# Performance work log

Hardware: AMD Instinct MI355X
Metric: run time of the kernel (lower is better)

## Reference

```python
import jax, jax.numpy as jnp
import numpy as np

BS, N, D, NC = 64, 512, 256, 4
REG = 0.5
N_ITER = 10
BIG = 1.0e9
LN_EPS = 1e-5


def _layer_norm(x, g, b):
    m = jnp.mean(x, axis=-1, keepdims=True)
    v = jnp.mean((x - m) ** 2, axis=-1, keepdims=True)
    return (x - m) * jax.lax.rsqrt(v + LN_EPS) * g + b


def _embed(x, W1, b1, g1, be1, W2, b2, g2, be2):
    h = _layer_norm(jax.nn.leaky_relu(x @ W1 + b1, 0.01), g1, be1)
    return _layer_norm(jax.nn.leaky_relu(h @ W2 + b2, 0.01), g2, be2)


def _one_hot_st(logits):
    # convert_one_hot(mode='max', hard=True, four_class=False, train): straight-through one-hot
    y = jax.nn.softmax(logits, axis=-1)
    y_hard = jax.nn.one_hot(jnp.argmax(y, axis=-1), logits.shape[-1], dtype=y.dtype)
    return jax.lax.stop_gradient(y_hard - y) + y


def _cdist(x, y):
    # torch.cdist p=2 (matmul form)
    sq = (jnp.sum(x * x, -1)[:, :, None] + jnp.sum(y * y, -1)[:, None, :]
          - 2.0 * jnp.einsum('bnd,bmd->bnm', x, y))
    return jnp.sqrt(jnp.maximum(sq, 0.0))


def _sinkhorn(a, b, C):
    # standard Sinkhorn-Knopp (POT sinkhorn_knopp), reg=REG, maxIter=N_ITER
    K = jnp.exp(-C / REG)
    def step(carry, _):
        u, v = carry
        v = b / (K.T @ u)
        u = a / (K @ v)
        return (u, v), None
    init = (jnp.full_like(a, 1.0 / a.shape[0]), jnp.full_like(b, 1.0 / b.shape[0]))
    (u, v), _ = jax.lax.scan(step, init, None, length=N_ITER)
    return u[:, None] * K * v[None, :]


def setup_inputs() -> dict:
    ks = jax.random.split(jax.random.key(0), 8)
    sc = 1.0 / np.sqrt(D)
    return {
        'case_A_logits': jax.random.normal(ks[0], (BS, N, NC), jnp.float32),
        'case_B_logits': jax.random.normal(ks[1], (BS, N, NC), jnp.float32),
        'case_A': jax.random.normal(ks[2], (BS, N, D), jnp.float32),
        'case_B': jax.random.normal(ks[3], (BS, N, D), jnp.float32),
        'relation_matrix': jax.random.uniform(ks[4], (BS, N, N), jnp.float32),
        'padding_mask_a': jnp.ones((BS, N), jnp.float32),
        'padding_mask_b': jnp.ones((BS, N), jnp.float32),
        'W1': jax.random.normal(ks[5], (D, D), jnp.float32) * sc,
        'b1': jnp.zeros((D,), jnp.float32),
        'g1': jnp.ones((D,), jnp.float32),
        'be1': jnp.zeros((D,), jnp.float32),
        'W2': jax.random.normal(ks[6], (D, D), jnp.float32) * sc,
        'b2': jnp.zeros((D,), jnp.float32),
        'g2': jnp.ones((D,), jnp.float32),
        'be2': jnp.zeros((D,), jnp.float32),
    }


def reference(case_A_logits, case_B_logits, case_A, case_B, relation_matrix,
              padding_mask_a, padding_mask_b,
              W1, b1, g1, be1, W2, b2, g2, be2):
    n = case_B_logits.shape[1]
    A1 = _one_hot_st(case_A_logits)                       # [bs, n, 4]
    B1 = _one_hot_st(case_B_logits)
    class_mask = jnp.einsum('bnc,bmc->bnm', A1, B1)       # [bs, n, n]
    pm = padding_mask_a[:, :, None] * padding_mask_b[:, None, :]
    pmv = -BIG * pm + BIG
    eA = _embed(case_A, W1, b1, g1, be1, W2, b2, g2, be2)
    eB = _embed(case_B, W1, b1, g1, be1, W2, b2, g2, be2)
    cost = _cdist(eA, eB)                                 # [bs, n, n]
    cost_class = cost + pmv                               # train path
    margin = jnp.full((n,), 1.0 / n, cost.dtype)
    plan = jax.vmap(lambda c: _sinkhorn(margin, margin, c))(cost_class)
    in_loss = jnp.mean(cost_class * class_mask * pm)
    out_loss = -jnp.mean(cost_class * (1.0 - class_mask) * pm)
    # simot branch: MSE criterion, simpercent=1.0 -> sim_mask all ones
    loss_raw = (plan * n - relation_matrix) ** 2
    sup_loss = jnp.sum(loss_raw * padding_mask_a[:, :, None]) / jnp.sum(padding_mask_a)
    return in_loss + out_loss + 10.0 * sup_loss
```

## Files before the change

### kernel.cpp

```cpp
#include <hip/hip_runtime.h>
#include <math.h>

#define BSZ 64
#define NPTS 512
#define DIM 256
#define MROWS 32768
#define TOTROWS 65536
#define BIGF 1.0e9f

typedef __bf16 bf16x8 __attribute__((ext_vector_type(8)));
typedef float  f32x4  __attribute__((ext_vector_type(4)));
typedef __attribute__((address_space(1))) const void* as1cv;
typedef __attribute__((address_space(3))) void* as3v;

#define KB_OFF    0ull
#define X_OFF     8388608ull
#define H_OFF     16777216ull
#define NORM_OFF  25165824ull
#define U_OFF     25231360ull
#define V_OFF     25264128ull
#define ARGA_OFF  25296896ull
#define ARGB_OFF  25329664ull
#define ACC_OFF   25362432ull
#define WT1_OFF   25362944ull
#define WT2_OFF   25395712ull

#define ACC_PA   0
#define ACC_IN   1
#define ACC_SUP  65
#define ACC_CNT  321

__device__ __forceinline__ float bf2f(unsigned short h) {
    return __uint_as_float(((unsigned int)h) << 16);
}
__device__ __forceinline__ unsigned short f2bf(float f) {
    unsigned int u = __float_as_uint(f);
    u = (u + 0x7FFFu + ((u >> 16) & 1u)) >> 16;
    return (unsigned short)u;
}

__device__ __forceinline__ float block_reduce_256(float val) {
    __shared__ float sh[4];
    int lane = threadIdx.x & 63;
    int wv = threadIdx.x >> 6;
    __syncthreads();
#pragma unroll
    for (int off = 32; off > 0; off >>= 1) val += __shfl_down(val, off, 64);
    if (lane == 0) sh[wv] = val;
    __syncthreads();
    float r = 0.f;
    if (wv == 0 && lane < 4) r = sh[lane];
    if (wv == 0) {
        r += __shfl_down(r, 2, 64);
        r += __shfl_down(r, 1, 64);
    }
    return r;
}

__device__ __forceinline__ void unpack8(uint4 w, float* k) {
    k[0] = __uint_as_float(w.x << 16);
    k[1] = __uint_as_float(w.x & 0xFFFF0000u);
    k[2] = __uint_as_float(w.y << 16);
    k[3] = __uint_as_float(w.y & 0xFFFF0000u);
    k[4] = __uint_as_float(w.z << 16);
    k[5] = __uint_as_float(w.z & 0xFFFF0000u);
    k[6] = __uint_as_float(w.w << 16);
    k[7] = __uint_as_float(w.w & 0xFFFF0000u);
}
__device__ __forceinline__ float dot8(const float* k, const float* vr) {
    float rs = k[0] * vr[0];
    rs = fmaf(k[1], vr[1], rs); rs = fmaf(k[2], vr[2], rs);
    rs = fmaf(k[3], vr[3], rs); rs = fmaf(k[4], vr[4], rs);
    rs = fmaf(k[5], vr[5], rs); rs = fmaf(k[6], vr[6], rs);
    return fmaf(k[7], vr[7], rs);
}

__device__ __forceinline__ float packed_reduce4(float p0, float p1, float p2, float p3, int l) {
    p0 += __shfl_xor(p0, 32, 64);
    p1 += __shfl_xor(p1, 32, 64);
    p2 += __shfl_xor(p2, 32, 64);
    p3 += __shfl_xor(p3, 32, 64);
    float m1 = (l & 32) ? p1 : p0;
    float m2 = (l & 32) ? p3 : p2;
    m1 += __shfl_xor(m1, 16, 64);
    m2 += __shfl_xor(m2, 16, 64);
    float s = (l & 16) ? m2 : m1;
    s += __shfl_xor(s, 8, 64);
    s += __shfl_xor(s, 4, 64);
    s += __shfl_xor(s, 2, 64);
    s += __shfl_xor(s, 1, 64);
    return s;
}
__device__ __forceinline__ float bcast_lane(float x, int lane) {
    return __uint_as_float((unsigned)__builtin_amdgcn_readlane((int)__float_as_uint(x), lane));
}

__global__ void zero_acc_kernel(float* acc, float* colsum) {
    int t = blockIdx.x * 256 + threadIdx.x;
    if (t < 512) acc[t] = 0.f;
    colsum[t] = 0.f;
}

__global__ __launch_bounds__(256) void argmax_pa_kernel(
    const float* __restrict__ la, const float* __restrict__ lb,
    const float* __restrict__ pa, int* __restrict__ argA, int* __restrict__ argB,
    float* __restrict__ acc) {
    int i = blockIdx.x * 256 + threadIdx.x;
    float4 a = *(const float4*)&la[(size_t)i * 4];
    float av[4] = {a.x, a.y, a.z, a.w};
    int ba = 0; float bv = av[0];
#pragma unroll
    for (int c = 1; c < 4; ++c) if (av[c] > bv) { bv = av[c]; ba = c; }
    argA[i] = ba;
    float4 b = *(const float4*)&lb[(size_t)i * 4];
    float bw[4] = {b.x, b.y, b.z, b.w};
    int bbi = 0; float bm = bw[0];
#pragma unroll
    for (int c = 1; c < 4; ++c) if (bw[c] > bm) { bm = bw[c]; bbi = c; }
    argB[i] = bbi;
    float p = pa[i];
#pragma unroll
    for (int off = 32; off > 0; off >>= 1) p += __shfl_down(p, off, 64);
    if ((threadIdx.x & 63) == 0) atomicAdd(&acc[ACC_PA], p);
}

__global__ __launch_bounds__(256) void cast_bf_kernel(
    const float* __restrict__ src, unsigned short* __restrict__ dst) {
    int tid = blockIdx.x * 256 + threadIdx.x;
#pragma unroll
    for (int k = 0; k < 4; ++k) {
        int i4 = tid + k * 524288;
        float4 v = *(const float4*)&src[(size_t)i4 * 4];
        ushort4 o;
        o.x = f2bf(v.x); o.y = f2bf(v.y); o.z = f2bf(v.z); o.w = f2bf(v.w);
        *(ushort4*)&dst[(size_t)i4 * 4] = o;
    }
}

__global__ __launch_bounds__(256) void cast_wt_kernel(
    const float* __restrict__ W, unsigned short* __restrict__ Wt) {
    __shared__ float tile[16][17];
    int tx = threadIdx.x & 15, ty = threadIdx.x >> 4;
    int bx = blockIdx.x, by = blockIdx.y;
    tile[ty][tx] = W[(size_t)(by * 16 + ty) * 256 + bx * 16 + tx];
    __syncthreads();
    Wt[(size_t)(bx * 16 + ty) * 256 + by * 16 + tx] = f2bf(tile[tx][ty]);
}

__global__ __launch_bounds__(256) void gemm_bf_kernel(
    const unsigned short* __restrict__ X, const unsigned short* __restrict__ Wt,
    unsigned short* __restrict__ Y) {
    __shared__ unsigned short As[64 * 256];
    __shared__ unsigned short Bs[64 * 256];
    const int t = threadIdx.x;
    const int L = t & 63, wv = t >> 6;
    const int q = L >> 4, n = L & 15;
    const size_t row0 = (size_t)blockIdx.x * 64;
    const int n0 = blockIdx.y * 64;
    {
        const int lrow = L >> 5;
        const int segp = L & 31;
#pragma unroll
        for (int j = 0; j < 8; ++j) {
            int row = wv * 16 + 2 * j + lrow;
            int sseg = segp ^ (row & 7);
            const unsigned short* ga = &X[(row0 + row) * 256 + sseg * 8];
            const unsigned short* gb = &Wt[(size_t)(n0 + row) * 256 + sseg * 8];
            __builtin_amdgcn_global_load_lds((as1cv)ga, (as3v)&As[(wv * 16 + 2 * j) * 256],
                                             16, 0, 0);
            __builtin_amdgcn_global_load_lds((as1cv)gb, (as3v)&Bs[(wv * 16 + 2 * j) * 256],
                                             16, 0, 0);
        }
    }
    f32x4 dot[4];
#pragma unroll
    for (int nt = 0; nt < 4; ++nt) dot[nt] = (f32x4){0.f, 0.f, 0.f, 0.f};
    __syncthreads();

    const int rowa = wv * 16 + n;
    const int sw = n & 7;
#pragma unroll
    for (int c = 0; c < 8; ++c) {
        bf16x8 av = *(const bf16x8*)&As[rowa * 256 + (((c * 4 + q) ^ sw) * 8)];
#pragma unroll
        for (int nt = 0; nt < 4; ++nt) {
            bf16x8 bv = *(const bf16x8*)&Bs[(nt * 16 + n) * 256 + (((c * 4 + q) ^ sw) * 8)];
            dot[nt] = __builtin_amdgcn_mfma_f32_16x16x32_bf16(av, bv, dot[nt], 0, 0, 0);
        }
    }
#pragma unroll
    for (int nt = 0; nt < 4; ++nt)
#pragma unroll
        for (int r = 0; r < 4; ++r) {
            size_t row = row0 + wv * 16 + q * 4 + r;
            Y[row * 256 + n0 + nt * 16 + n] = f2bf(dot[nt][r]);
        }
}

__global__ __launch_bounds__(256) void ln_bf_kernel(
    const unsigned short* __restrict__ Yin, unsigned short* __restrict__ Yout,
    const float* __restrict__ bias, const float* __restrict__ gam,
    const float* __restrict__ bet, float* __restrict__ norms) {
    int lane = threadIdx.x & 63;
    int wv = threadIdx.x >> 6;
    size_t row = (size_t)blockIdx.x * 4 + wv;
    ushort4 y4 = *(const ushort4*)&Yin[row * 256 + lane * 4];
    float4 b4 = *(const float4*)&bias[lane * 4];
    float h[4] = {bf2f(y4.x) + b4.x, bf2f(y4.y) + b4.y, bf2f(y4.z) + b4.z, bf2f(y4.w) + b4.w};
#pragma unroll
    for (int e = 0; e < 4; ++e) h[e] = h[e] >= 0.f ? h[e] : 0.01f * h[e];
    float s = h[0] + h[1] + h[2] + h[3];
    float sq = h[0] * h[0] + h[1] * h[1] + h[2] * h[2] + h[3] * h[3];
#pragma unroll
    for (int off = 32; off > 0; off >>= 1) {
        s += __shfl_down(s, off, 64);
        sq += __shfl_down(sq, off, 64);
    }
    s = __shfl(s, 0, 64); sq = __shfl(sq, 0, 64);
    float mean = s * (1.f / 256.f);
    float var = fmaxf(sq * (1.f / 256.f) - mean * mean, 0.f);
    float inv = rsqrtf(var + 1e-5f);
    float4 g4 = *(const float4*)&gam[lane * 4];
    float4 e4 = *(const float4*)&bet[lane * 4];
    float gv[4] = {g4.x, g4.y, g4.z, g4.w};
    float ev[4] = {e4.x, e4.y, e4.z, e4.w};
    ushort4 o4; float nr = 0.f;
    {
        unsigned short ob[4];
#pragma unroll
        for (int e = 0; e < 4; ++e) {
            float o = (h[e] - mean) * inv * gv[e] + ev[e];
            ob[e] = f2bf(o);
            float orr = bf2f(ob[e]);
            nr += orr * orr;
        }
        o4.x = ob[0]; o4.y = ob[1]; o4.z = ob[2]; o4.w = ob[3];
    }
    *(ushort4*)&Yout[row * 256 + lane * 4] = o4;
    if (norms) {
#pragma unroll
        for (int off = 32; off > 0; off >>= 1) nr += __shfl_down(nr, off, 64);
        if (lane == 0) norms[row] = nr;
    }
}

__global__ __launch_bounds__(512) void cost_mfma_kernel(
    const unsigned short* __restrict__ E, const float* __restrict__ norms,
    const int* __restrict__ argA, const int* __restrict__ argB,
    const float* __restrict__ pa, const float* __restrict__ pb,
    unsigned short* __restrict__ Kb16, float* __restrict__ acc,
    float* __restrict__ colsum) {
    __shared__ unsigned short As[64 * 256];
    __shared__ unsigned short Bs[2][64 * 256];
    __shared__ float cswave[8][256];
    __shared__ float redp[8];
    const int t = threadIdx.x;
    const int L = t & 63, wv = t >> 6;
    const int q = L >> 4, n = L & 15;
    const int rh = wv & 3, ch = wv >> 2;
    const int b = blockIdx.x & 63;
    const int i0 = (blockIdx.x >> 6) * 64;
    const unsigned short* eA = E + (size_t)b * 512 * 256;
    const unsigned short* eB = E + (size_t)(32768 + b * 512) * 256;
    const int lrow = L >> 5, segp = L & 31;

#pragma unroll
    for (int jj = 0; jj < 4; ++jj) {
        int row = wv * 8 + 2 * jj + lrow;
        int sseg = segp ^ (row & 7);
        __builtin_amdgcn_global_load_lds((as1cv)&eA[(size_t)(i0 + row) * 256 + sseg * 8],
                                         (as3v)&As[(wv * 8 + 2 * jj) * 256], 16, 0, 0);
        __builtin_amdgcn_global_load_lds((as1cv)&eB[(size_t)row * 256 + sseg * 8],
                                         (as3v)&Bs[0][(wv * 8 + 2 * jj) * 256], 16, 0, 0);
    }
    const int base_row = i0 + rh * 16 + q * 4;
    float nA[4], pAr[4]; int cA[4];
#pragma unroll
    for (int rr = 0; rr < 4; ++rr) {
        nA[rr] = norms[b * 512 + base_row + rr];
        pAr[rr] = pa[b * 512 + base_row + rr];
        cA[rr] = argA[b * 512 + base_row + rr];
    }
    float part = 0.f;
    __syncthreads();

    const int rowa = rh * 16 + n;
    const int sw = n & 7;
    bf16x8 areg[8];
#pragma unroll
    for (int c = 0; c < 8; ++c)
        areg[c] = *(const bf16x8*)&As[rowa * 256 + (((c * 4 + q) ^ sw) * 8)];

    for (int j = 0; j < 8; ++j) {
        const int cur = j & 1;
        if (j < 7) {
#pragma unroll
            for (int jj = 0; jj < 4; ++jj) {
                int row = wv * 8 + 2 * jj + lrow;
                int sseg = segp ^ (row & 7);
                __builtin_amdgcn_global_load_lds(
                    (as1cv)&eB[(size_t)((j + 1) * 64 + row) * 256 + sseg * 8],
                    (as3v)&Bs[cur ^ 1][(wv * 8 + 2 * jj) * 256], 16, 0, 0);
            }
        }
        f32x4 dot[2];
        dot[0] = (f32x4){0.f, 0.f, 0.f, 0.f};
        dot[1] = (f32x4){0.f, 0.f, 0.f, 0.f};
#pragma unroll
        for (int c = 0; c < 8; ++c) {
#pragma unroll
            for (int np = 0; np < 2; ++np) {
                int nt = ch * 2 + np;
                bf16x8 bv = *(const bf16x8*)&Bs[cur][(nt * 16 + n) * 256 +
                                                     (((c * 4 + q) ^ sw) * 8)];
                dot[np] = __builtin_amdgcn_mfma_f32_16x16x32_bf16(areg[c], bv, dot[np], 0, 0, 0);
            }
        }
#pragma unroll
        for (int np = 0; np < 2; ++np) {
            int nt = ch * 2 + np;
            int col = j * 64 + nt * 16 + n;
            float nB = norms[32768 + b * 512 + col];
            float pB = pb[b * 512 + col];
            int cB = argB[b * 512 + col];
            float cloc = 0.f;
#pragma unroll
            for (int rr = 0; rr < 4; ++rr) {
                float d2 = nA[rr] + nB - 2.f * dot[np][rr];
                float c = sqrtf(fmaxf(d2, 0.f));
                float pm = pAr[rr] * pB;
                float cc = c + (BIGF - BIGF * pm);
                float sgn = (cA[rr] == cB) ? 1.f : -1.f;
                part += cc * sgn * pm;
                unsigned short kb = f2bf(expf(-2.f * cc));
                Kb16[((size_t)b * 512 + base_row + rr) * 512 + col] = kb;
                cloc += bf2f(kb);
            }
            cloc += __shfl_xor(cloc, 16, 64);
            cloc += __shfl_xor(cloc, 32, 64);
            if (L < 16) cswave[wv][j * 32 + np * 16 + L] = cloc;
        }
        __syncthreads();
    }

    {
        float pw = part;
#pragma unroll
        for (int off = 32; off > 0; off >>= 1) pw += __shfl_down(pw, off, 64);
        if (L == 0) redp[wv] = pw;
    }
    __syncthreads();
    {
        int c = t & 511;
        int local = ((c >> 6) << 5) | (c & 31);
        int cch = (c >> 5) & 1;
        float s = cswave[4 * cch][local] + cswave[4 * cch + 1][local] +
                  cswave[4 * cch + 2][local] + cswave[4 * cch + 3][local];
        atomicAdd(&colsum[(size_t)b * 512 + c], s);
    }
    if (t == 0) {
        float s = 0.f;
#pragma unroll
        for (int k = 0; k < 8; ++k) s += redp[k];
        atomicAdd(&acc[ACC_IN + b], s);
    }
}

__global__ __launch_bounds__(1024) void sinkhorn_kernel(
    const unsigned short* __restrict__ Kb16, const float* __restrict__ colsum,
    float* __restrict__ v) {
    const int b = blockIdx.x;
    const unsigned short* Kb = Kb16 + (size_t)b * 262144;
    __shared__ float vv[512];
    __shared__ float cp[16][512];
    const int t = threadIdx.x, wv = t >> 6, l = t & 63;
    const unsigned short* base = Kb + (size_t)(wv * 32) * 512 + l * 8;

    if (t < 512) vv[t] = 1.f / colsum[(size_t)b * 512 + t];
    __syncthreads();

    for (int it = 1; it <= 9; ++it) {
        float vr[8];
        *(f32x4*)&vr[0] = *(const f32x4*)&vv[l * 8];
        *(f32x4*)&vr[4] = *(const f32x4*)&vv[l * 8 + 4];
        float cs[8];
#pragma unroll
        for (int e = 0; e < 8; ++e) cs[e] = 0.f;
#pragma unroll 2
        for (int g = 0; g < 8; ++g) {
            const unsigned short* gb = base + (size_t)(g * 4) * 512;
            uint4 w0 = *(const uint4*)(gb);
            uint4 w1 = *(const uint4*)(gb + 512);
            uint4 w2 = *(const uint4*)(gb + 1024);
            uint4 w3 = *(const uint4*)(gb + 1536);
            float k0[8], k1[8], k2[8], k3[8];
            unpack8(w0, k0); unpack8(w1, k1); unpack8(w2, k2); unpack8(w3, k3);
            float p0 = dot8(k0, vr);
            float p1 = dot8(k1, vr);
            float p2 = dot8(k2, vr);
            float p3 = dot8(k3, vr);
            float s = packed_reduce4(p0, p1, p2, p3, l);
            float us = 0.001953125f * __builtin_amdgcn_rcpf(s);
            float uA = bcast_lane(us, 0);
            float uC = bcast_lane(us, 16);
            float uB = bcast_lane(us, 32);
            float uD = bcast_lane(us, 48);
#pragma unroll
            for (int e = 0; e < 8; ++e) {
                float c = fmaf(k0[e], uA, cs[e]);
                c = fmaf(k1[e], uB, c);
                c = fmaf(k2[e], uC, c);
                cs[e] = fmaf(k3[e], uD, c);
            }
        }
        *(f32x4*)&cp[wv][l * 8]     = *(f32x4*)&cs[0];
        *(f32x4*)&cp[wv][l * 8 + 4] = *(f32x4*)&cs[4];
        __syncthreads();
        if (t < 512) {
            float ss = 0.f;
#pragma unroll
            for (int k = 0; k < 16; ++k) ss += cp[k][t];
            vv[t] = (1.f / 512.f) / ss;
        }
        __syncthreads();
    }
    if (t < 512) v[(size_t)b * 512 + t] = vv[t];
}

__global__ __launch_bounds__(256) void sup_kernel(
    const unsigned short* __restrict__ Kb16, const float* __restrict__ v,
    const float* __restrict__ rel, const float* __restrict__ pa,
    float* __restrict__ acc) {
    const int b = blockIdx.x >> 6;
    const int rg = blockIdx.x & 63;
    const int t = threadIdx.x;
    const int h = t >> 5;
    const int c = t & 31;
    const int row = rg * 8 + h;
    const unsigned int* kp =
        (const unsigned int*)(Kb16 + ((size_t)b * 512 + row) * 512 + c * 16);
    uint4 kw0 = *(const uint4*)(kp);
    uint4 kw1 = *(const uint4*)(kp + 4);
    float k[16];
    unpack8(kw0, k); unpack8(kw1, k + 8);
    float vr[16];
    *(f32x4*)&vr[0]  = *(const f32x4*)&v[b * 512 + c * 16];
    *(f32x4*)&vr[4]  = *(const f32x4*)&v[b * 512 + c * 16 + 4];
    *(f32x4*)&vr[8]  = *(const f32x4*)&v[b * 512 + c * 16 + 8];
    *(f32x4*)&vr[12] = *(const f32x4*)&v[b * 512 + c * 16 + 12];
    float rs = 0.f;
#pragma unroll
    for (int e = 0; e < 16; ++e) rs = fmaf(k[e], vr[e], rs);
#pragma unroll
    for (int off = 16; off > 0; off >>= 1) rs += __shfl_xor(rs, off, 32);
    float inv = 1.f / rs;
    float part = 0.f;
    const float* rp = &rel[((size_t)b * 512 + row) * 512 + c * 16];
#pragma unroll
    for (int e = 0; e < 16; e += 4) {
        float4 r4 = *(const float4*)(rp + e);
        float d0 = k[e]     * vr[e]     * inv - r4.x;
        float d1 = k[e + 1] * vr[e + 1] * inv - r4.y;
        float d2 = k[e + 2] * vr[e + 2] * inv - r4.z;
        float d3 = k[e + 3] * vr[e + 3] * inv - r4.w;
        part += d0 * d0 + d1 * d1 + d2 * d2 + d3 * d3;
    }
    part *= pa[b * 512 + row];
    float tot = block_reduce_256(part);
    if (t == 0) atomicAdd(&acc[ACC_SUP + (blockIdx.x & 255)], tot);
}

__global__ __launch_bounds__(256) void final_kernel(const float* __restrict__ acc,
                                                    float* __restrict__ out) {
    int t = threadIdx.x;
    float vin = (t < 64) ? acc[ACC_IN + t] : 0.f;
    float sIn = block_reduce_256(vin);
    float vsup = acc[ACC_SUP + t];
    float sSup = block_reduce_256(vsup);
    if (t == 0)
        out[0] = sIn * (1.f / 16777216.f) + 10.f * sSup / acc[ACC_PA];
}

extern "C" void kernel_launch(void* const* d_in, const int* in_sizes, int n_in,
                              void* d_out, int out_size, void* d_ws, size_t ws_size,
                              hipStream_t stream) {
    const float* la  = (const float*)d_in[0];
    const float* lb  = (const float*)d_in[1];
    const float* xA  = (const float*)d_in[2];
    const float* xB  = (const float*)d_in[3];
    const float* rel = (const float*)d_in[4];
    const float* pa  = (const float*)d_in[5];
    const float* pb  = (const float*)d_in[6];
    const float* W1  = (const float*)d_in[7];
    const float* b1  = (const float*)d_in[8];
    const float* g1  = (const float*)d_in[9];
    const float* be1 = (const float*)d_in[10];
    const float* W2  = (const float*)d_in[11];
    const float* b2  = (const float*)d_in[12];
    const float* g2  = (const float*)d_in[13];
    const float* be2 = (const float*)d_in[14];
    float* out = (float*)d_out;

    float* ws = (float*)d_ws;
    unsigned short* Kb16 = (unsigned short*)(ws + KB_OFF);
    unsigned short* Xbf  = (unsigned short*)(ws + X_OFF);
    unsigned short* Hbf  = (unsigned short*)(ws + H_OFF);
    float* norms = ws + NORM_OFF;
    float* u     = ws + U_OFF;
    float* v     = ws + V_OFF;
    int* argA    = (int*)(ws + ARGA_OFF);
    int* argB    = (int*)(ws + ARGB_OFF);
    float* acc   = ws + ACC_OFF;
    unsigned short* Wt1 = (unsigned short*)(ws + WT1_OFF);
    unsigned short* Wt2 = (unsigned short*)(ws + WT2_OFF);

    zero_acc_kernel<<<128, 256, 0, stream>>>(acc, u);
    argmax_pa_kernel<<<128, 256, 0, stream>>>(la, lb, pa, argA, argB, acc);

    cast_bf_kernel<<<2048, 256, 0, stream>>>(xA, Xbf);
    cast_bf_kernel<<<2048, 256, 0, stream>>>(xB, Xbf + (size_t)MROWS * DIM);
    cast_wt_kernel<<<dim3(16, 16), 256, 0, stream>>>(W1, Wt1);
    cast_wt_kernel<<<dim3(16, 16), 256, 0, stream>>>(W2, Wt2);

    gemm_bf_kernel<<<dim3(1024, 4), 256, 0, stream>>>(Xbf, Wt1, Kb16);
    ln_bf_kernel<<<16384, 256, 0, stream>>>(Kb16, Hbf, b1, g1, be1, nullptr);
    gemm_bf_kernel<<<dim3(1024, 4), 256, 0, stream>>>(Hbf, Wt2, Kb16);
    ln_bf_kernel<<<16384, 256, 0, stream>>>(Kb16, Xbf, b2, g2, be2, norms);

    cost_mfma_kernel<<<512, 512, 0, stream>>>(Xbf, norms, argA, argB, pa, pb,
                                              Kb16, acc, u);

    sinkhorn_kernel<<<64, 1024, 0, stream>>>(Kb16, u, v);

    sup_kernel<<<4096, 256, 0, stream>>>(Kb16, v, rel, pa, acc);
    final_kernel<<<1, 256, 0, stream>>>(acc, out);
}
```

Measured before the change: 386.8 us.

## Fuse embedding GEMM with bias, leaky-ReLU and LayerNorm epilogue

Replaces the separate bf16 GEMM and LayerNorm kernels with one kernel. It keeps the full 256x256 transposed weight in LDS, computes full output rows per wave with MFMA, and applies bias, leaky-ReLU, LayerNorm and the norm computation in registers. This removes the bf16 intermediate round trip through global memory and two kernel launches per layer. The trade-offs are a large 128KB LDS footprint, a single block per CU with only 256 blocks, many accumulator registers, and uncoalesced 2-byte scattered output stores.

```diff
diff --git a/kernel.cpp b/kernel.cpp
--- a/kernel.cpp
+++ b/kernel.cpp
@@ -147,100 +147,94 @@
     Wt[(size_t)(bx * 16 + ty) * 256 + by * 16 + tx] = f2bf(tile[tx][ty]);
 }
 
-__global__ __launch_bounds__(256) void gemm_bf_kernel(
+__global__ __launch_bounds__(512) void gemmln_kernel(
     const unsigned short* __restrict__ X, const unsigned short* __restrict__ Wt,
-    unsigned short* __restrict__ Y) {
-    __shared__ unsigned short As[64 * 256];
-    __shared__ unsigned short Bs[64 * 256];
+    const float* __restrict__ bias, const float* __restrict__ gam,
+    const float* __restrict__ bet,
+    unsigned short* __restrict__ Yout, float* __restrict__ norms) {
+    __shared__ unsigned short Ws[256 * 256];
     const int t = threadIdx.x;
     const int L = t & 63, wv = t >> 6;
     const int q = L >> 4, n = L & 15;
-    const size_t row0 = (size_t)blockIdx.x * 64;
-    const int n0 = blockIdx.y * 64;
     {
-        const int lrow = L >> 5;
-        const int segp = L & 31;
-#pragma unroll
-        for (int j = 0; j < 8; ++j) {
-            int row = wv * 16 + 2 * j + lrow;
+        const int lrow = L >> 5, segp = L & 31;
+#pragma unroll
+        for (int j = 0; j < 16; ++j) {
+            int row = wv * 32 + 2 * j + lrow;
             int sseg = segp ^ (row & 7);
-            const unsigned short* ga = &X[(row0 + row) * 256 + sseg * 8];
-            const unsigned short* gb = &Wt[(size_t)(n0 + row) * 256 + sseg * 8];
-            __builtin_amdgcn_global_load_lds((as1cv)ga, (as3v)&As[(wv * 16 + 2 * j) * 256],
-                                             16, 0, 0);
-            __builtin_amdgcn_global_load_lds((as1cv)gb, (as3v)&Bs[(wv * 16 + 2 * j) * 256],
-                                             16, 0, 0);
-        }
-    }
-    f32x4 dot[4];
-#pragma unroll
-    for (int nt = 0; nt < 4; ++nt) dot[nt] = (f32x4){0.f, 0.f, 0.f, 0.f};
-    __syncthreads();
-
-    const int rowa = wv * 16 + n;
+            __builtin_amdgcn_global_load_lds((as1cv)&Wt[(size_t)row * 256 + sseg * 8],
+                                             (as3v)&Ws[(wv * 32 + 2 * j) * 256], 16, 0, 0);
+        }
+    }
+    float bcol[16], gcol[16], ecol[16];
+#pragma unroll
+    for (int nt = 0; nt < 16; ++nt) {
+        bcol[nt] = bias[nt * 16 + n];
+        gcol[nt] = gam[nt * 16 + n];
+        ecol[nt] = bet[nt * 16 + n];
+    }
+    __syncthreads();
+
     const int sw = n & 7;
-#pragma unroll
-    for (int c = 0; c < 8; ++c) {
-        bf16x8 av = *(const bf16x8*)&As[rowa * 256 + (((c * 4 + q) ^ sw) * 8)];
-#pragma unroll
-        for (int nt = 0; nt < 4; ++nt) {
-            bf16x8 bv = *(const bf16x8*)&Bs[(nt * 16 + n) * 256 + (((c * 4 + q) ^ sw) * 8)];
-            dot[nt] = __builtin_amdgcn_mfma_f32_16x16x32_bf16(av, bv, dot[nt], 0, 0, 0);
-        }
-    }
-#pragma unroll
-    for (int nt = 0; nt < 4; ++nt)
+    for (int p = 0; p < 2; ++p) {
+        const size_t row0 = (size_t)blockIdx.x * 256 + p * 128 + wv * 16;
+        bf16x8 a[8];
+#pragma unroll
+        for (int ks = 0; ks < 8; ++ks)
+            a[ks] = *(const bf16x8*)&X[(row0 + n) * 256 + ks * 32 + q * 8];
+        f32x4 acc[16];
+#pragma unroll
+        for (int nt = 0; nt < 16; ++nt) acc[nt] = (f32x4){0.f, 0.f, 0.f, 0.f};
+#pragma unroll
+        for (int nt = 0; nt < 16; ++nt) {
+#pragma unroll
+            for (int ks = 0; ks < 8; ++ks) {
+                bf16x8 bv = *(const bf16x8*)&Ws[(nt * 16 + n) * 256 +
+                                                (((ks * 4 + q) ^ sw) * 8)];
+                acc[nt] = __builtin_amdgcn_mfma_f32_16x16x32_bf16(a[ks], bv, acc[nt], 0, 0, 0);
+            }
+        }
+        float mean4[4], inv4[4];
 #pragma unroll
         for (int r = 0; r < 4; ++r) {
-            size_t row = row0 + wv * 16 + q * 4 + r;
-            Y[row * 256 + n0 + nt * 16 + n] = f2bf(dot[nt][r]);
-        }
-}
-
-__global__ __launch_bounds__(256) void ln_bf_kernel(
-    const unsigned short* __restrict__ Yin, unsigned short* __restrict__ Yout,
-    const float* __restrict__ bias, const float* __restrict__ gam,
-    const float* __restrict__ bet, float* __restrict__ norms) {
-    int lane = threadIdx.x & 63;
-    int wv = threadIdx.x >> 6;
-    size_t row = (size_t)blockIdx.x * 4 + wv;
-    ushort4 y4 = *(const ushort4*)&Yin[row * 256 + lane * 4];
-    float4 b4 = *(const float4*)&bias[lane * 4];
-    float h[4] = {bf2f(y4.x) + b4.x, bf2f(y4.y) + b4.y, bf2f(y4.z) + b4.z, bf2f(y4.w) + b4.w};
-#pragma unroll
-    for (int e = 0; e < 4; ++e) h[e] = h[e] >= 0.f ? h[e] : 0.01f * h[e];
-    float s = h[0] + h[1] + h[2] + h[3];
-    float sq = h[0] * h[0] + h[1] * h[1] + h[2] * h[2] + h[3] * h[3];
-#pragma unroll
-    for (int off = 32; off > 0; off >>= 1) {
-        s += __shfl_down(s, off, 64);
-        sq += __shfl_down(sq, off, 64);
-    }
-    s = __shfl(s, 0, 64); sq = __shfl(sq, 0, 64);
-    float mean = s * (1.f / 256.f);
-    float var = fmaxf(sq * (1.f / 256.f) - mean * mean, 0.f);
-    float inv = rsqrtf(var + 1e-5f);
-    float4 g4 = *(const float4*)&gam[lane * 4];
-    float4 e4 = *(const float4*)&bet[lane * 4];
-    float gv[4] = {g4.x, g4.y, g4.z, g4.w};
-    float ev[4] = {e4.x, e4.y, e4.z, e4.w};
-    ushort4 o4; float nr = 0.f;
-    {
-        unsigned short ob[4];
-#pragma unroll
-        for (int e = 0; e < 4; ++e) {
-            float o = (h[e] - mean) * inv * gv[e] + ev[e];
-            ob[e] = f2bf(o);
-            float orr = bf2f(ob[e]);
-            nr += orr * orr;
-        }
-        o4.x = ob[0]; o4.y = ob[1]; o4.z = ob[2]; o4.w = ob[3];
-    }
-    *(ushort4*)&Yout[row * 256 + lane * 4] = o4;
-    if (norms) {
-#pragma unroll
-        for (int off = 32; off > 0; off >>= 1) nr += __shfl_down(nr, off, 64);
-        if (lane == 0) norms[row] = nr;
+            float s = 0.f, sq = 0.f;
+#pragma unroll
+            for (int nt = 0; nt < 16; ++nt) {
+                float h = acc[nt][r] + bcol[nt];
+                h = h >= 0.f ? h : 0.01f * h;
+                acc[nt][r] = h;
+                s += h; sq += h * h;
+            }
+#pragma unroll
+            for (int m = 1; m < 16; m <<= 1) {
+                s += __shfl_xor(s, m, 64);
+                sq += __shfl_xor(sq, m, 64);
+            }
+            float mean = s * (1.f / 256.f);
+            float var = fmaxf(sq * (1.f / 256.f) - mean * mean, 0.f);
+            mean4[r] = mean;
+            inv4[r] = rsqrtf(var + 1e-5f);
+        }
+        float nr[4] = {0.f, 0.f, 0.f, 0.f};
+#pragma unroll
+        for (int nt = 0; nt < 16; ++nt) {
+#pragma unroll
+            for (int r = 0; r < 4; ++r) {
+                float o = (acc[nt][r] - mean4[r]) * inv4[r] * gcol[nt] + ecol[nt];
+                unsigned short ob = f2bf(o);
+                float of = bf2f(ob);
+                nr[r] += of * of;
+                Yout[(row0 + q * 4 + r) * 256 + nt * 16 + n] = ob;
+            }
+        }
+        if (norms) {
+#pragma unroll
+            for (int r = 0; r < 4; ++r) {
+#pragma unroll
+                for (int m = 1; m < 16; m <<= 1) nr[r] += __shfl_xor(nr[r], m, 64);
+                if (n == 0) norms[row0 + q * 4 + r] = nr[r];
+            }
+        }
     }
 }
 
@@ -522,10 +516,8 @@
     cast_wt_kernel<<<dim3(16, 16), 256, 0, stream>>>(W1, Wt1);
     cast_wt_kernel<<<dim3(16, 16), 256, 0, stream>>>(W2, Wt2);
 
-    gemm_bf_kernel<<<dim3(1024, 4), 256, 0, stream>>>(Xbf, Wt1, Kb16);
-    ln_bf_kernel<<<16384, 256, 0, stream>>>(Kb16, Hbf, b1, g1, be1, nullptr);
-    gemm_bf_kernel<<<dim3(1024, 4), 256, 0, stream>>>(Hbf, Wt2, Kb16);
-    ln_bf_kernel<<<16384, 256, 0, stream>>>(Kb16, Xbf, b2, g2, be2, norms);
+    gemmln_kernel<<<256, 512, 0, stream>>>(Xbf, Wt1, b1, g1, be1, Hbf, nullptr);
+    gemmln_kernel<<<256, 512, 0, stream>>>(Hbf, Wt2, b2, g2, be2, Xbf, norms);
 
     cost_mfma_kernel<<<512, 512, 0, stream>>>(Xbf, norms, argA, argB, pa, pb,
                                               Kb16, acc, u);
```

Result: faster. 363.3 us (-6.1%).
